# Optimization experiments

Hardware: AMD Instinct MI355X
Metric: run time of the kernel (lower is better)

## Reference

```python
import jax, jax.numpy as jnp
import numpy as np

EMBED_DIM = 1024
NUM_HEADS = 16
HEAD_DIM = EMBED_DIM // NUM_HEADS
RANK = 512
B, S = 4, 4096


def setup_inputs() -> dict:
    key = jax.random.key(0)
    ks = jax.random.split(key, 16)
    sd = 0.02
    inp = {
        "query": jax.random.normal(ks[0], (B, S, EMBED_DIM), jnp.float32),
        "key": jax.random.normal(ks[1], (B, S, EMBED_DIM), jnp.float32),
        "value": jax.random.normal(ks[2], (B, S, EMBED_DIM), jnp.float32),
        # torch nn.Linear weights: [out_features, in_features]
        "q_down_w": jax.random.normal(ks[3], (RANK, EMBED_DIM), jnp.float32) * sd,
        "q_up_w": jax.random.normal(ks[4], (EMBED_DIM, RANK), jnp.float32) * sd,
        "q_up_b": jax.random.normal(ks[5], (EMBED_DIM,), jnp.float32) * sd,
        "k_down_w": jax.random.normal(ks[6], (RANK, EMBED_DIM), jnp.float32) * sd,
        "k_up_w": jax.random.normal(ks[7], (EMBED_DIM, RANK), jnp.float32) * sd,
        "k_up_b": jax.random.normal(ks[8], (EMBED_DIM,), jnp.float32) * sd,
        "v_down_w": jax.random.normal(ks[9], (RANK, EMBED_DIM), jnp.float32) * sd,
        "v_up_w": jax.random.normal(ks[10], (EMBED_DIM, RANK), jnp.float32) * sd,
        "v_up_b": jax.random.normal(ks[11], (EMBED_DIM,), jnp.float32) * sd,
        "out_w": jax.random.normal(ks[12], (EMBED_DIM, EMBED_DIM), jnp.float32) * sd,
        "out_b": jax.random.normal(ks[13], (EMBED_DIM,), jnp.float32) * sd,
    }
    return inp


def _linear(x, w, b=None):
    y = x @ w.T
    return y if b is None else y + b


def reference(query, key, value,
              q_down_w, q_up_w, q_up_b,
              k_down_w, k_up_w, k_up_b,
              v_down_w, v_up_w, v_up_b,
              out_w, out_b):
    b, s, _ = query.shape
    # low-rank QKV projections
    q = _linear(_linear(query, q_down_w), q_up_w, q_up_b)
    k = _linear(_linear(key, k_down_w), k_up_w, k_up_b)
    v = _linear(_linear(value, v_down_w), v_up_w, v_up_b)
    # [B,S,E] -> [B,H,S,Dh]
    q = q.reshape(b, s, NUM_HEADS, HEAD_DIM).transpose(0, 2, 1, 3)
    k = k.reshape(b, s, NUM_HEADS, HEAD_DIM).transpose(0, 2, 1, 3)
    v = v.reshape(b, s, NUM_HEADS, HEAD_DIM).transpose(0, 2, 1, 3)
    # kernel feature map: elu + 1  (note: scaling_factor in original is computed but unused)
    q = jax.nn.elu(q) + 1.0
    k = jax.nn.elu(k) + 1.0
    k_sum = k.sum(axis=-2)                              # [B,H,Dh]
    denom = jnp.einsum('bhnd,bhd->bhn', q, k_sum)       # [B,H,S]
    kv = jnp.einsum('bhnd,bhne->bhde', k, v)            # [B,H,Dh,Dh]
    num = jnp.einsum('bhnd,bhde->bhne', q, kv)          # [B,H,S,Dh]
    out = num / (denom[..., None] + 1e-6)
    out = out.transpose(0, 2, 1, 3).reshape(b, s, EMBED_DIM)
    return _linear(out, out_w, out_b)
```

## Files before the change

### kernel.cpp

```cpp
#include <hip/hip_runtime.h>
#include <hip/hip_bf16.h>

typedef unsigned short ushort_t;
typedef unsigned int uint_t;
typedef __attribute__((ext_vector_type(8))) short short8;
typedef __attribute__((ext_vector_type(4))) float f32x4;

#define EMBED 1024
#define RANK  512
#define BB    4
#define SS    4096
#define HH    16
#define DHD   64
#define MM    (BB*SS)
#define NCHUNK 16

__device__ __forceinline__ float bf2f(ushort_t u) {
    union { uint_t i; float f; } v; v.i = ((uint_t)u) << 16; return v.f;
}
__device__ __forceinline__ ushort_t f2bf(float f) {
    union { float f; uint_t i; } v; v.f = f;
    uint_t r = v.i + 0x7FFFu + ((v.i >> 16) & 1u);
    return (ushort_t)(r >> 16);
}
__device__ __forceinline__ void gl2lds16(const void* g, void* l) {
    __builtin_amdgcn_global_load_lds((const __attribute__((address_space(1))) void*)g,
                                     (__attribute__((address_space(3))) void*)l,
                                     16, 0, 0);
}

template<int EPI>
__global__ __launch_bounds__(256) void gemm_bt(
    const ushort_t* __restrict__ A0, const ushort_t* __restrict__ A1, const ushort_t* __restrict__ A2,
    const ushort_t* __restrict__ B0, const ushort_t* __restrict__ B1, const ushort_t* __restrict__ B2,
    const float* __restrict__ bias0, const float* __restrict__ bias1, const float* __restrict__ bias2,
    void* __restrict__ C0, void* __restrict__ C1, void* __restrict__ C2,
    int N, int K, int nbx)
{
    __shared__ __align__(16) ushort_t As[2][128 * 32];
    __shared__ __align__(16) ushort_t Bs[2][128 * 32];

    const int z = blockIdx.z;
    const ushort_t* Ab   = (z == 0) ? A0 : (z == 1) ? A1 : A2;
    const ushort_t* Bm   = (z == 0) ? B0 : (z == 1) ? B1 : B2;
    const float*    bias = (z == 0) ? bias0 : (z == 1) ? bias1 : bias2;
    void*           Cv   = (z == 0) ? C0 : (z == 1) ? C1 : C2;

    const int cpx = gridDim.x >> 3;
    const int bid = blockIdx.x;
    const int wg  = (bid & 7) * cpx + (bid >> 3);
    const long m0 = (long)(wg / nbx) * 128;
    const long n0 = (long)(wg % nbx) * 128;

    const int t = threadIdx.x;
    const int lane = t & 63;
    const int w = t >> 6;
    const int wr = (w >> 1) * 64;
    const int wc = (w & 1) * 64;
    const int fr = lane & 15;
    const int kq = (lane >> 4) * 8;

    const int srow = t >> 2;
    const int scol = ((t & 3) ^ ((srow >> 1) & 3)) * 8;

    const int kqs = (((kq >> 3) ^ ((fr >> 1) & 3))) * 8;

    f32x4 acc[4][4] = {};

    auto STAGE = [&](int k0, int buf) {
        #pragma unroll
        for (int ro = 0; ro < 2; ++ro) {
            const int row = ro * 64 + srow;
            gl2lds16(Ab + (m0 + row) * (long)K + k0 + scol,
                     (char*)As[buf] + (ro * 256 + w * 64) * 16);
            gl2lds16(Bm + (n0 + row) * (long)K + k0 + scol,
                     (char*)Bs[buf] + (ro * 256 + w * 64) * 16);
        }
    };

    STAGE(0, 0);
    __syncthreads();

    int cur = 0;
    const int nt = K >> 5;
    for (int ti = 0; ti < nt; ++ti) {
        if (ti + 1 < nt) STAGE((ti + 1) << 5, cur ^ 1);

        short8 av[4], bv[4];
        #pragma unroll
        for (int mi = 0; mi < 4; ++mi)
            av[mi] = *(const short8*)&As[cur][(wr + mi * 16 + fr) * 32 + kqs];
        #pragma unroll
        for (int nf = 0; nf < 4; ++nf)
            bv[nf] = *(const short8*)&Bs[cur][(wc + nf * 16 + fr) * 32 + kqs];
        #pragma unroll
        for (int mi = 0; mi < 4; ++mi)
            #pragma unroll
            for (int nf = 0; nf < 4; ++nf)
                acc[mi][nf] = __builtin_amdgcn_mfma_f32_16x16x32_bf16(
                    av[mi], bv[nf], acc[mi][nf], 0, 0, 0);

        __syncthreads();
        cur ^= 1;
    }

    ushort_t* Cb = (ushort_t*)Cv;
    float*    Cf = (float*)Cv;
    const int rj = (lane >> 4) * 4;
    const bool do_elu = (EPI == 2) && (z < 2);
    #pragma unroll
    for (int nf = 0; nf < 4; ++nf) {
        const long col = n0 + wc + nf * 16 + fr;
        const float bval = (EPI >= 2) ? bias[col] : 0.0f;
        #pragma unroll
        for (int mi = 0; mi < 4; ++mi) {
            #pragma unroll
            for (int j = 0; j < 4; ++j) {
                const long row = m0 + wr + mi * 16 + rj + j;
                float x = acc[mi][nf][j];
                if (EPI >= 2) x += bval;
                if (do_elu) x = (x > 0.0f) ? (x + 1.0f) : __expf(x);
                if (EPI == 3) Cf[row * (long)N + col] = x;
                else          Cb[row * (long)N + col] = f2bf(x);
            }
        }
    }
}

__global__ __launch_bounds__(256) void cvt_act(const float* __restrict__ q,
                                               const float* __restrict__ k,
                                               const float* __restrict__ v,
                                               ushort_t* __restrict__ qo,
                                               ushort_t* __restrict__ ko,
                                               ushort_t* __restrict__ vo)
{
    const int zz = blockIdx.y;
    const float* src = (zz == 0) ? q : (zz == 1) ? k : v;
    ushort_t*    dst = (zz == 0) ? qo : (zz == 1) ? ko : vo;
    const long i = ((long)blockIdx.x * 256 + threadIdx.x) * 8;
    f32x4 f0 = *(const f32x4*)(src + i);
    f32x4 f1 = *(const f32x4*)(src + i + 4);
    short8 h;
    h[0] = (short)f2bf(f0[0]); h[1] = (short)f2bf(f0[1]);
    h[2] = (short)f2bf(f0[2]); h[3] = (short)f2bf(f0[3]);
    h[4] = (short)f2bf(f1[0]); h[5] = (short)f2bf(f1[1]);
    h[6] = (short)f2bf(f1[2]); h[7] = (short)f2bf(f1[3]);
    *(short8*)(dst + i) = h;
}

__global__ __launch_bounds__(256) void cvt_weights(
    const float* __restrict__ s0, const float* __restrict__ s1,
    const float* __restrict__ s2, const float* __restrict__ s3,
    const float* __restrict__ s4, const float* __restrict__ s5,
    const float* __restrict__ s6,
    ushort_t* __restrict__ d0, ushort_t* __restrict__ d1,
    ushort_t* __restrict__ d2, ushort_t* __restrict__ d3,
    ushort_t* __restrict__ d4, ushort_t* __restrict__ d5,
    ushort_t* __restrict__ d6)
{
    const int y = blockIdx.y;
    const float* src; ushort_t* dst; int n;
    switch (y) {
        case 0: src = s0; dst = d0; n = RANK * EMBED; break;
        case 1: src = s1; dst = d1; n = RANK * EMBED; break;
        case 2: src = s2; dst = d2; n = RANK * EMBED; break;
        case 3: src = s3; dst = d3; n = RANK * EMBED; break;
        case 4: src = s4; dst = d4; n = RANK * EMBED; break;
        case 5: src = s5; dst = d5; n = RANK * EMBED; break;
        default: src = s6; dst = d6; n = EMBED * EMBED; break;
    }
    const int i = (blockIdx.x * 256 + threadIdx.x) * 4;
    if (i < n) {
        f32x4 f = *(const f32x4*)(src + i);
        typedef __attribute__((ext_vector_type(4))) short short4v;
        short4v h;
        h[0] = (short)f2bf(f[0]); h[1] = (short)f2bf(f[1]);
        h[2] = (short)f2bf(f[2]); h[3] = (short)f2bf(f[3]);
        *(short4v*)(dst + i) = h;
    }
}

__global__ __launch_bounds__(256) void kv_stats(const ushort_t* __restrict__ Kp,
                                                const ushort_t* __restrict__ Vp,
                                                float* __restrict__ kvp,
                                                float* __restrict__ ksump)
{
    __shared__ __align__(16) ushort_t Ks[64 * 64];
    __shared__ __align__(16) ushort_t Vs[64 * 64];
    const int t = threadIdx.x;
    const int w = t >> 6;
    const int bh = blockIdx.x;
    const int chunk = blockIdx.y;
    const int b = bh >> 4, h = bh & 15;
    const int d0 = (t & 15) * 4;
    const int e0 = (t >> 4) * 4;
    float acc[4][4] = {};
    float sks[4] = {};
    const long hbase = ((long)b * SS) * EMBED + h * DHD;

    for (int sub = 0; sub < 4; ++sub) {
        const int n00 = chunk * 256 + sub * 64;
        #pragma unroll
        for (int ro = 0; ro < 2; ++ro) {
            const int idx = ro * 256 + t;
            const int r = idx >> 3, c16 = idx & 7;
            const long g = hbase + (long)(n00 + r) * EMBED + c16 * 8;
            gl2lds16(Kp + g, (char*)Ks + (ro * 256 + w * 64) * 16);
            gl2lds16(Vp + g, (char*)Vs + (ro * 256 + w * 64) * 16);
        }
        __syncthreads();
        #pragma unroll 8
        for (int n = 0; n < 64; ++n) {
            const uint_t* kr = (const uint_t*)(Ks + n * 64 + d0);
            const uint_t* vr = (const uint_t*)(Vs + n * 64 + e0);
            const uint_t k01 = kr[0], k23 = kr[1];
            const uint_t v01 = vr[0], v23 = vr[1];
            float kd[4], ve[4];
            {
                union { uint_t i; float f; } a, bq, c, dq;
                a.i = k01 << 16; bq.i = k01 & 0xffff0000u;
                c.i = k23 << 16; dq.i = k23 & 0xffff0000u;
                kd[0] = a.f; kd[1] = bq.f; kd[2] = c.f; kd[3] = dq.f;
            }
            {
                union { uint_t i; float f; } a, bq, c, dq;
                a.i = v01 << 16; bq.i = v01 & 0xffff0000u;
                c.i = v23 << 16; dq.i = v23 & 0xffff0000u;
                ve[0] = a.f; ve[1] = bq.f; ve[2] = c.f; ve[3] = dq.f;
            }
            #pragma unroll
            for (int e = 0; e < 4; ++e)
                #pragma unroll
                for (int d = 0; d < 4; ++d)
                    acc[e][d] += ve[e] * kd[d];
            if (e0 == 0) {
                #pragma unroll
                for (int d = 0; d < 4; ++d) sks[d] += kd[d];
            }
        }
        __syncthreads();
    }

    float* dst = kvp + ((long)chunk * 64 + bh) * 4096;
    #pragma unroll
    for (int e = 0; e < 4; ++e) {
        f32x4 vv; vv[0] = acc[e][0]; vv[1] = acc[e][1]; vv[2] = acc[e][2]; vv[3] = acc[e][3];
        *(f32x4*)(dst + (e0 + e) * 64 + d0) = vv;
    }
    if (e0 == 0) {
        float* sd = ksump + ((long)chunk * 64 + bh) * 64 + d0;
        #pragma unroll
        for (int d = 0; d < 4; ++d) sd[d] = sks[d];
    }
}

__global__ __launch_bounds__(256) void kv_reduce(const float* __restrict__ kvp,
                                                 const float* __restrict__ ksump,
                                                 ushort_t* __restrict__ kvb,
                                                 float* __restrict__ ksumf)
{
    const int bh = blockIdx.x;
    const int t = threadIdx.x;
    const long base = (long)bh * 4096 + t * 16;
    f32x4 s[4] = {};
    #pragma unroll 4
    for (int c = 0; c < NCHUNK; ++c) {
        const float* src = kvp + (long)c * 64 * 4096 + base;
        #pragma unroll
        for (int j = 0; j < 4; ++j) s[j] += *(const f32x4*)(src + j * 4);
    }
    short8 o0, o1;
    #pragma unroll
    for (int j = 0; j < 4; ++j) {
        o0[j]     = (short)f2bf(s[0][j]); o0[4 + j] = (short)f2bf(s[1][j]);
        o1[j]     = (short)f2bf(s[2][j]); o1[4 + j] = (short)f2bf(s[3][j]);
    }
    *(short8*)(kvb + base)     = o0;
    *(short8*)(kvb + base + 8) = o1;

    if (t < 64) {
        float ss = 0.f;
        #pragma unroll
        for (int c = 0; c < NCHUNK; ++c) ss += ksump[(long)c * 64 * 64 + bh * 64 + t];
        ksumf[bh * 64 + t] = ss;
    }
}

__global__ __launch_bounds__(256) void attn_out(const ushort_t* __restrict__ Qp,
                                                const ushort_t* __restrict__ kvb,
                                                const float* __restrict__ ksum,
                                                ushort_t* __restrict__ Op)
{
    __shared__ __align__(16) ushort_t Qs[128 * 64];
    __shared__ __align__(16) ushort_t KVs[64 * 64];
    __shared__ float kss[64];
    __shared__ float dnm[128];
    const int t = threadIdx.x;
    const int w = t >> 6, lane = t & 63;
    const int bh = blockIdx.x, mc = blockIdx.y;
    const int b = bh >> 4, h = bh & 15;
    const long base = ((long)b * SS + mc * 128) * EMBED + h * DHD;

    #pragma unroll
    for (int ro = 0; ro < 4; ++ro) {
        const int idx = ro * 256 + t;
        const int r = idx >> 3, c16 = idx & 7;
        gl2lds16(Qp + base + (long)r * EMBED + c16 * 8,
                 (char*)Qs + (ro * 256 + w * 64) * 16);
    }
    #pragma unroll
    for (int ro = 0; ro < 2; ++ro) {
        const int idx = ro * 256 + t;
        gl2lds16(kvb + (long)bh * 4096 + idx * 8,
                 (char*)KVs + (ro * 256 + w * 64) * 16);
    }
    if (t < 64) kss[t] = ksum[bh * 64 + t];
    __syncthreads();

    if (t < 128) {
        float s = 0.f;
        const uint_t* qr = (const uint_t*)(Qs + t * 64);
        #pragma unroll
        for (int jj = 0; jj < 32; ++jj) {
            const uint_t u = qr[jj];
            union { uint_t i; float f; } lo, hi;
            lo.i = u << 16; hi.i = u & 0xffff0000u;
            s += lo.f * kss[2 * jj] + hi.f * kss[2 * jj + 1];
        }
        dnm[t] = s;
    }

    const int fr = lane & 15, kq = (lane >> 4) * 8;
    f32x4 acc[2][4] = {};
    #pragma unroll
    for (int ks = 0; ks < 2; ++ks) {
        short8 av[2], bv[4];
        #pragma unroll
        for (int mi = 0; mi < 2; ++mi)
            av[mi] = *(const short8*)&Qs[(w * 32 + mi * 16 + fr) * 64 + ks * 32 + kq];
        #pragma unroll
        for (int nf = 0; nf < 4; ++nf)
            bv[nf] = *(const short8*)&KVs[(nf * 16 + fr) * 64 + ks * 32 + kq];
        #pragma unroll
        for (int mi = 0; mi < 2; ++mi)
            #pragma unroll
            for (int nf = 0; nf < 4; ++nf)
                acc[mi][nf] = __builtin_amdgcn_mfma_f32_16x16x32_bf16(
                    av[mi], bv[nf], acc[mi][nf], 0, 0, 0);
    }
    __syncthreads();

    const int rj = (lane >> 4) * 4;
    #pragma unroll
    for (int mi = 0; mi < 2; ++mi) {
        #pragma unroll
        for (int nf = 0; nf < 4; ++nf) {
            #pragma unroll
            for (int j = 0; j < 4; ++j) {
                const int r = w * 32 + mi * 16 + rj + j;
                const int c = nf * 16 + fr;
                const float x = acc[mi][nf][j] / (dnm[r] + 1e-6f);
                Op[base + (long)r * EMBED + c] = f2bf(x);
            }
        }
    }
}

extern "C" void kernel_launch(void* const* d_in, const int* in_sizes, int n_in,
                              void* d_out, int out_size, void* d_ws, size_t ws_size,
                              hipStream_t stream)
{
    (void)in_sizes; (void)n_in; (void)out_size; (void)ws_size;
    const float* query = (const float*)d_in[0];
    const float* key_  = (const float*)d_in[1];
    const float* value = (const float*)d_in[2];
    const float* q_dw  = (const float*)d_in[3];
    const float* q_uw  = (const float*)d_in[4];
    const float* q_ub  = (const float*)d_in[5];
    const float* k_dw  = (const float*)d_in[6];
    const float* k_uw  = (const float*)d_in[7];
    const float* k_ub  = (const float*)d_in[8];
    const float* v_dw  = (const float*)d_in[9];
    const float* v_uw  = (const float*)d_in[10];
    const float* v_ub  = (const float*)d_in[11];
    const float* o_w   = (const float*)d_in[12];
    const float* o_b   = (const float*)d_in[13];

    char* ws = (char*)d_ws;
    size_t off = 0;
    auto alloc = [&](size_t bytes) -> void* {
        void* p = ws + off;
        off += (bytes + 255) & ~(size_t)255;
        return p;
    };
    const size_t WSMALL = (size_t)RANK * EMBED;
    ushort_t* bw_qd = (ushort_t*)alloc(WSMALL * 2);
    ushort_t* bw_qu = (ushort_t*)alloc(WSMALL * 2);
    ushort_t* bw_kd = (ushort_t*)alloc(WSMALL * 2);
    ushort_t* bw_ku = (ushort_t*)alloc(WSMALL * 2);
    ushort_t* bw_vd = (ushort_t*)alloc(WSMALL * 2);
    ushort_t* bw_vu = (ushort_t*)alloc(WSMALL * 2);
    ushort_t* bw_o  = (ushort_t*)alloc((size_t)EMBED * EMBED * 2);
    ushort_t* Qb    = (ushort_t*)alloc((size_t)MM * EMBED * 2);
    ushort_t* Kb    = (ushort_t*)alloc((size_t)MM * EMBED * 2);
    ushort_t* Vb    = (ushort_t*)alloc((size_t)MM * EMBED * 2);
    ushort_t* Y1q   = (ushort_t*)alloc((size_t)MM * RANK * 2);
    ushort_t* Y1k   = (ushort_t*)alloc((size_t)MM * RANK * 2);
    ushort_t* Y1v   = (ushort_t*)alloc((size_t)MM * RANK * 2);
    float*    ksump = (float*)alloc((size_t)NCHUNK * 64 * 64 * 4);
    float*    ksumf = (float*)alloc((size_t)64 * 64 * 4);
    ushort_t* kvb   = (ushort_t*)alloc((size_t)64 * 64 * 64 * 2);

    ushort_t* PQ = Qb;
    ushort_t* PK = Kb;
    ushort_t* PV = Vb;
    float*    kvp = (float*)Y1q;
    ushort_t* O   = Y1k;

    const dim3 blk(256);

    cvt_act<<<dim3((size_t)MM * EMBED / 2048, 3), blk, 0, stream>>>(
        query, key_, value, Qb, Kb, Vb);
    cvt_weights<<<dim3(EMBED * EMBED / 1024, 7), blk, 0, stream>>>(
        q_dw, q_uw, k_dw, k_uw, v_dw, v_uw, o_w,
        bw_qd, bw_qu, bw_kd, bw_ku, bw_vd, bw_vu, bw_o);

    gemm_bt<0><<<dim3(MM / 128 * (RANK / 128), 1, 3), blk, 0, stream>>>(
        Qb, Kb, Vb,
        bw_qd, bw_kd, bw_vd,
        nullptr, nullptr, nullptr,
        Y1q, Y1k, Y1v,
        RANK, EMBED, RANK / 128);

    gemm_bt<2><<<dim3(MM / 128 * (EMBED / 128), 1, 3), blk, 0, stream>>>(
        Y1q, Y1k, Y1v,
        bw_qu, bw_ku, bw_vu,
        q_ub, k_ub, v_ub,
        PQ, PK, PV,
        EMBED, RANK, EMBED / 128);

    kv_stats<<<dim3(64, NCHUNK), blk, 0, stream>>>(PK, PV, kvp, ksump);
    kv_reduce<<<dim3(64), blk, 0, stream>>>(kvp, ksump, kvb, ksumf);
    attn_out<<<dim3(64, 32), blk, 0, stream>>>(PQ, kvb, ksumf, O);

    gemm_bt<3><<<dim3(MM / 128 * (EMBED / 128), 1, 1), blk, 0, stream>>>(
        O, nullptr, nullptr,
        bw_o, nullptr, nullptr,
        o_b, nullptr, nullptr,
        d_out, nullptr, nullptr,
        EMBED, EMBED, EMBED / 128);
}
```

Measured before the change: 332.6 us.

## Triple-buffer GEMM LDS pipeline and stage bf16 epilogue through LDS

The GEMM mainloop moves from double buffering to a three-stage LDS ring. It prefetches two tiles ahead and waits with explicit vmcnt waits plus a single barrier per iteration, where it used to sync once per iteration after compute. For bf16 outputs, the epilogue now writes results to LDS and then stores 16-byte vectorized rows to global memory instead of scattered 2-byte stores. This raises LDS use to 48KB, which may lower occupancy, and depends on correct vmcnt counting for the asynchronous loads.

```diff
diff --git a/kernel.cpp b/kernel.cpp
--- a/kernel.cpp
+++ b/kernel.cpp
@@ -37,8 +37,7 @@
     void* __restrict__ C0, void* __restrict__ C1, void* __restrict__ C2,
     int N, int K, int nbx)
 {
-    __shared__ __align__(16) ushort_t As[2][128 * 32];
-    __shared__ __align__(16) ushort_t Bs[2][128 * 32];
+    __shared__ __align__(16) char lds_raw[49152];
 
     const int z = blockIdx.z;
     const ushort_t* Ab   = (z == 0) ? A0 : (z == 1) ? A1 : A2;
@@ -62,37 +61,45 @@
 
     const int srow = t >> 2;
     const int scol = ((t & 3) ^ ((srow >> 1) & 3)) * 8;
-
     const int kqs = (((kq >> 3) ^ ((fr >> 1) & 3))) * 8;
 
-    f32x4 acc[4][4] = {};
-
     auto STAGE = [&](int k0, int buf) {
+        char* Ad = lds_raw + buf * 8192;
+        char* Bd = lds_raw + 24576 + buf * 8192;
         #pragma unroll
         for (int ro = 0; ro < 2; ++ro) {
             const int row = ro * 64 + srow;
-            gl2lds16(Ab + (m0 + row) * (long)K + k0 + scol,
-                     (char*)As[buf] + (ro * 256 + w * 64) * 16);
-            gl2lds16(Bm + (n0 + row) * (long)K + k0 + scol,
-                     (char*)Bs[buf] + (ro * 256 + w * 64) * 16);
+            gl2lds16(Ab + (m0 + row) * (long)K + k0 + scol, Ad + (ro * 256 + w * 64) * 16);
+            gl2lds16(Bm + (n0 + row) * (long)K + k0 + scol, Bd + (ro * 256 + w * 64) * 16);
         }
     };
 
+    f32x4 acc[4][4] = {};
+    const int nt = K >> 5;
+
     STAGE(0, 0);
-    __syncthreads();
+    STAGE(32, 1);
 
     int cur = 0;
-    const int nt = K >> 5;
     for (int ti = 0; ti < nt; ++ti) {
-        if (ti + 1 < nt) STAGE((ti + 1) << 5, cur ^ 1);
-
+        if (ti + 1 < nt) { asm volatile("s_waitcnt vmcnt(4)" ::: "memory"); }
+        else             { asm volatile("s_waitcnt vmcnt(0)" ::: "memory"); }
+        __builtin_amdgcn_sched_barrier(0);
+        __builtin_amdgcn_s_barrier();
+        __builtin_amdgcn_sched_barrier(0);
+
+        int nb = cur + 2; if (nb >= 3) nb -= 3;
+        if (ti + 2 < nt) STAGE((ti + 2) << 5, nb);
+
+        const ushort_t* Asc = (const ushort_t*)(lds_raw + cur * 8192);
+        const ushort_t* Bsc = (const ushort_t*)(lds_raw + 24576 + cur * 8192);
         short8 av[4], bv[4];
         #pragma unroll
         for (int mi = 0; mi < 4; ++mi)
-            av[mi] = *(const short8*)&As[cur][(wr + mi * 16 + fr) * 32 + kqs];
+            av[mi] = *(const short8*)&Asc[(wr + mi * 16 + fr) * 32 + kqs];
         #pragma unroll
         for (int nf = 0; nf < 4; ++nf)
-            bv[nf] = *(const short8*)&Bs[cur][(wc + nf * 16 + fr) * 32 + kqs];
+            bv[nf] = *(const short8*)&Bsc[(wc + nf * 16 + fr) * 32 + kqs];
         #pragma unroll
         for (int mi = 0; mi < 4; ++mi)
             #pragma unroll
@@ -100,29 +107,51 @@
                 acc[mi][nf] = __builtin_amdgcn_mfma_f32_16x16x32_bf16(
                     av[mi], bv[nf], acc[mi][nf], 0, 0, 0);
 
+        ++cur; if (cur == 3) cur = 0;
+    }
+
+    const int rj = (lane >> 4) * 4;
+    if (EPI == 3) {
+        float* Cf = (float*)Cv;
         __syncthreads();
-        cur ^= 1;
-    }
-
-    ushort_t* Cb = (ushort_t*)Cv;
-    float*    Cf = (float*)Cv;
-    const int rj = (lane >> 4) * 4;
-    const bool do_elu = (EPI == 2) && (z < 2);
-    #pragma unroll
-    for (int nf = 0; nf < 4; ++nf) {
-        const long col = n0 + wc + nf * 16 + fr;
-        const float bval = (EPI >= 2) ? bias[col] : 0.0f;
-        #pragma unroll
-        for (int mi = 0; mi < 4; ++mi) {
-            #pragma unroll
-            for (int j = 0; j < 4; ++j) {
-                const long row = m0 + wr + mi * 16 + rj + j;
-                float x = acc[mi][nf][j];
-                if (EPI >= 2) x += bval;
-                if (do_elu) x = (x > 0.0f) ? (x + 1.0f) : __expf(x);
-                if (EPI == 3) Cf[row * (long)N + col] = x;
-                else          Cb[row * (long)N + col] = f2bf(x);
+        #pragma unroll
+        for (int nf = 0; nf < 4; ++nf) {
+            const long col = n0 + wc + nf * 16 + fr;
+            const float bval = bias[col];
+            #pragma unroll
+            for (int mi = 0; mi < 4; ++mi)
+                #pragma unroll
+                for (int j = 0; j < 4; ++j)
+                    Cf[(m0 + wr + mi * 16 + rj + j) * (long)N + col] = acc[mi][nf][j] + bval;
+        }
+    } else {
+        ushort_t* Ct = (ushort_t*)lds_raw;
+        __syncthreads();
+        const bool do_elu = (EPI == 2) && (z < 2);
+        #pragma unroll
+        for (int nf = 0; nf < 4; ++nf) {
+            const int coll = wc + nf * 16 + fr;
+            const float bval = (EPI >= 2) ? bias[n0 + coll] : 0.0f;
+            #pragma unroll
+            for (int mi = 0; mi < 4; ++mi) {
+                #pragma unroll
+                for (int j = 0; j < 4; ++j) {
+                    float x = acc[mi][nf][j];
+                    if (EPI >= 2) x += bval;
+                    if (do_elu) x = (x > 0.0f) ? (x + 1.0f) : __expf(x);
+                    Ct[(wr + mi * 16 + rj + j) * 128 + coll] = f2bf(x);
+                }
             }
+        }
+        __syncthreads();
+        ushort_t* Cb = (ushort_t*)Cv;
+        #pragma unroll
+        for (int it = 0; it < 8; ++it) {
+            const int idx = it * 256 + t;
+            const int r   = idx >> 4;
+            const int c8  = (idx & 15) * 8;
+            short8 vv = *(const short8*)&Ct[r * 128 + c8];
+            *(short8*)(Cb + (m0 + r) * (long)N + n0 + c8) = vv;
         }
     }
 }
```

After: 299.8 us. 1.11x faster.
